# Performance work log

Measured on AMD Instinct MI355X. Metric: run time of the kernel, lower is better.

The kernel has to match this reference:

```python
import jax, jax.numpy as jnp
import numpy as np

N_BITS = 32
HIDDEN = 128


def _neighborhoods(z):
    """z: (B,k,H,W) -> (B,k,9,H,W) 3x3 neighborhoods (zero-padded), center zeroed.

    Position ordering matches F.unfold(kernel_size=3): row-major over (di,dj),
    so index 4 is the center, which the module masks to 0.
    """
    B, k, H, W = z.shape
    zp = jnp.pad(z, ((0, 0), (0, 0), (1, 1), (1, 1)))
    views = []
    for di in range(3):
        for dj in range(3):
            if di == 1 and dj == 1:  # center masked out
                views.append(jnp.zeros_like(z))
            else:
                views.append(zp[:, :, di:di + H, dj:dj + W])
    return jnp.stack(views, axis=2)  # (B,k,9,H,W)


def setup_inputs() -> dict:
    key = jax.random.key(0)
    k1, k2, k3, k4, k5 = jax.random.split(key, 5)
    B, k, H, W = 8, N_BITS, 256, 256
    z = jax.random.normal(k1, (B, k, H, W), dtype=jnp.float32)
    # nn.Linear(9*k, hidden): weight (hidden, 9k), feature order = k-outer, 9-inner
    W1 = jax.random.normal(k2, (HIDDEN, 9 * k), dtype=jnp.float32) * (1.0 / np.sqrt(9 * k))
    b1 = jax.random.normal(k3, (HIDDEN,), dtype=jnp.float32) * 0.01
    W2 = jax.random.normal(k4, (k, HIDDEN), dtype=jnp.float32) * (1.0 / np.sqrt(HIDDEN))
    b2 = jax.random.normal(k5, (k,), dtype=jnp.float32) * 0.01
    return {"z": z, "W1": W1, "b1": b1, "W2": W2, "b2": b2}


def reference(z, W1, b1, W2, b2):
    B, k, H, W = z.shape
    win = _neighborhoods(z)                      # (B,k,9,H,W)
    W1r = W1.reshape(HIDDEN, k, 9)               # split (9k) -> (k,9), k-outer
    h = jnp.einsum('bkphw,dkp->bdhw', win, W1r) + b1[None, :, None, None]
    h = jax.nn.relu(h)
    logits = jnp.einsum('bdhw,kd->bkhw', h, W2) + b2[None, :, None, None]
    return logits  # (B,k,H,W)
```

## Files before the change

kernel.cpp:

```cpp
#include <hip/hip_runtime.h>


#define KC 32
#define HH 256
#define WW 256
#define HID 128
#define YS 8
#define ZROW 2640

typedef __attribute__((ext_vector_type(8))) short short8;
typedef __attribute__((ext_vector_type(4))) float f32x4;

__device__ __forceinline__ unsigned short f2bf(float f) {
    union { float f; unsigned int i; } x; x.f = f;
    unsigned int r = x.i + 0x7FFFu + ((x.i >> 16) & 1u);
    return (unsigned short)(r >> 16);
}

__global__ void prep_weights(const float* __restrict__ w1,
                             const float* __restrict__ w2,
                             unsigned short* __restrict__ w1t,
                             unsigned short* __restrict__ w2t) {
    int i = blockIdx.x * 256 + threadIdx.x;
    if (i < 9 * HID * KC) {
        int c = i & 31;
        int d = (i >> 5) & 127;
        int p = i >> 12;
        w1t[i] = f2bf(w1[d * (9 * KC) + c * 9 + p]);
    } else if (i < 9 * HID * KC + KC * HID) {
        int j = i - 9 * HID * KC;
        w2t[j] = f2bf(w2[j]);
    }
}

__global__ __launch_bounds__(256) void local_pred_kernel(
    const float* __restrict__ zg,
    const unsigned short* __restrict__ w1t,
    const float* __restrict__ b1g,
    const unsigned short* __restrict__ w2t,
    const float* __restrict__ b2g,
    float* __restrict__ outg)
{
    __shared__ __attribute__((aligned(16))) unsigned short z_lds[3 * ZROW];
    __shared__ __attribute__((aligned(16))) unsigned short h_lds[64 * 136];

    const int tid = threadIdx.x;
    const int l   = tid & 63;
    const int o   = tid >> 6;
    const int bidx = blockIdx.x;
    const int x0 = (bidx & 3) << 6;
    const int y0 = ((bidx >> 2) & 31) * YS;
    const int b  = bidx >> 7;

    const int wave = tid >> 6;
    const int lane = tid & 63;
    const int lr = lane & 15;
    const int lq = lane >> 4;
    const int wm = wave >> 1;
    const int wn = wave & 1;

    const float* zb = zg + (size_t)b * KC * HH * WW;

    float bias1[4];
#pragma unroll
    for (int nt = 0; nt < 4; ++nt) bias1[nt] = b1g[wn * 64 + nt * 16 + lr];
    float bias2[2];
#pragma unroll
    for (int nt = 0; nt < 2; ++nt) bias2[nt] = b2g[nt * 16 + lr];
    short8 w2f[4][2];
#pragma unroll
    for (int k4 = 0; k4 < 4; ++k4)
#pragma unroll
        for (int nt = 0; nt < 2; ++nt)
            w2f[k4][nt] = *(const short8*)&w2t[(nt * 16 + lr) * HID + k4 * 32 + lq * 8];

    const int aoff0 = (wm * 32 + lr) * 40 + lq * 8;
    const int bbase = (wn * 64 + lr) * KC + lq * 8;
    const int m2    = wave * 16 + lr;

    const int ho    = tid >> 1;
    const int hside = tid & 1;
    const int hgx   = x0 - 1 + hside * 65;
    const bool hgx_ok = (unsigned)hgx < (unsigned)WW;

    int sA = (y0 + 2) % 3, sB = y0 % 3, sC = (y0 + 1) % 3;

    {
        int slots[3] = {sA, sB, sC};
#pragma unroll
        for (int dy = 0; dy < 3; ++dy) {
            int gy = y0 - 1 + dy;
            int slot = slots[dy];
            bool rowok = (unsigned)gy < (unsigned)HH;
            float m8[8];
            const float* p = zb + ((o * 8) * HH + gy) * WW + x0 + l;
#pragma unroll
            for (int j = 0; j < 8; ++j) m8[j] = rowok ? p[j * HH * WW] : 0.f;
            union { short8 s; unsigned int u[4]; } w;
            union { float f; unsigned int i; } uu[8];
#pragma unroll
            for (int j = 0; j < 8; ++j) uu[j].f = m8[j];
#pragma unroll
            for (int k = 0; k < 4; ++k)
                w.u[k] = __builtin_amdgcn_perm(uu[2 * k + 1].i, uu[2 * k].i, 0x07060302u);
            *(short8*)&z_lds[(slot * 66 + l + 1) * 40 + o * 8] = w.s;
            if (tid < 8) {
                bool ok = rowok && hgx_ok;
                float e8[8];
                const float* q = zb + ((ho * 8) * HH + gy) * WW + hgx;
#pragma unroll
                for (int j = 0; j < 8; ++j) e8[j] = ok ? q[j * HH * WW] : 0.f;
                union { short8 s; unsigned int u[4]; } we;
                union { float f; unsigned int i; } ue[8];
#pragma unroll
                for (int j = 0; j < 8; ++j) ue[j].f = e8[j];
#pragma unroll
                for (int k = 0; k < 4; ++k)
                    we.u[k] = __builtin_amdgcn_perm(ue[2 * k + 1].i, ue[2 * k].i, 0x07060302u);
                *(short8*)&z_lds[(slot * 66 + hside * 65) * 40 + ho * 8] = we.s;
            }
        }
    }

    const int tap_di[8] = {0, 0, 0, 1, 1, 2, 2, 2};
    const int tap_dj[8] = {0, 1, 2, 0, 2, 0, 1, 2};

    for (int r = 0; r < YS; ++r) {
        const int y = y0 + r;
        __syncthreads();

        f32x4 acc[2][4];
#pragma unroll
        for (int mt = 0; mt < 2; ++mt)
#pragma unroll
            for (int nt = 0; nt < 4; ++nt)
                acc[mt][nt] = (f32x4){0.f, 0.f, 0.f, 0.f};

        const int rowoff[3] = {sA * ZROW, sB * ZROW, sC * ZROW};
#pragma unroll
        for (int t = 0; t < 8; ++t) {
            const int di = tap_di[t], dj = tap_dj[t];
            const int abase = rowoff[di] + dj * 40 + aoff0;
            short8 afr[2];
            afr[0] = *(const short8*)&z_lds[abase];
            afr[1] = *(const short8*)&z_lds[abase + 16 * 40];
            const int p = di * 3 + dj;
#pragma unroll
            for (int nt = 0; nt < 4; ++nt) {
                short8 bfr = *(const short8*)&w1t[p * (HID * KC) + nt * 512 + bbase];
#pragma unroll
                for (int mt = 0; mt < 2; ++mt)
                    acc[mt][nt] = __builtin_amdgcn_mfma_f32_16x16x32_bf16(
                        afr[mt], bfr, acc[mt][nt], 0, 0, 0);
            }
        }

#pragma unroll
        for (int nt = 0; nt < 4; ++nt) {
            int d = wn * 64 + nt * 16 + lr;
#pragma unroll
            for (int mt = 0; mt < 2; ++mt) {
#pragma unroll
                for (int rr = 0; rr < 4; ++rr) {
                    float v = acc[mt][nt][rr] + bias1[nt];
                    v = v > 0.f ? v : 0.f;
                    int m = wm * 32 + mt * 16 + lq * 4 + rr;
                    h_lds[m * 136 + d] = f2bf(v);
                }
            }
        }
        __syncthreads();

        const bool dostage = (r < YS - 1);
        const int gy = y + 2;
        const bool rowok = dostage && ((unsigned)gy < (unsigned)HH);
        float m8[8], e8[8];
        {
            const float* p = zb + ((o * 8) * HH + gy) * WW + x0 + l;
#pragma unroll
            for (int j = 0; j < 8; ++j) m8[j] = rowok ? p[j * HH * WW] : 0.f;
            bool ok = rowok && hgx_ok && (tid < 8);
            const float* q = zb + ((ho * 8) * HH + gy) * WW + hgx;
#pragma unroll
            for (int j = 0; j < 8; ++j) e8[j] = ok ? q[j * HH * WW] : 0.f;
        }

        f32x4 acc2[2];
        acc2[0] = (f32x4){0.f, 0.f, 0.f, 0.f};
        acc2[1] = (f32x4){0.f, 0.f, 0.f, 0.f};
#pragma unroll
        for (int k4 = 0; k4 < 4; ++k4) {
            short8 afr = *(const short8*)&h_lds[m2 * 136 + k4 * 32 + lq * 8];
#pragma unroll
            for (int nt = 0; nt < 2; ++nt)
                acc2[nt] = __builtin_amdgcn_mfma_f32_16x16x32_bf16(afr, w2f[k4][nt],
                                                                   acc2[nt], 0, 0, 0);
        }

#pragma unroll
        for (int nt = 0; nt < 2; ++nt) {
            int kout = nt * 16 + lr;
            f32x4 pack;
#pragma unroll
            for (int rr = 0; rr < 4; ++rr) pack[rr] = acc2[nt][rr] + bias2[nt];
            int mb = wave * 16 + lq * 4;
            size_t off = ((size_t)(b * KC + kout) * HH + y) * WW + x0 + mb;
            *(f32x4*)&outg[off] = pack;
        }

        if (dostage) {
            union { short8 s; unsigned int u[4]; } w;
            union { float f; unsigned int i; } uu[8];
#pragma unroll
            for (int j = 0; j < 8; ++j) uu[j].f = m8[j];
#pragma unroll
            for (int k = 0; k < 4; ++k)
                w.u[k] = __builtin_amdgcn_perm(uu[2 * k + 1].i, uu[2 * k].i, 0x07060302u);
            *(short8*)&z_lds[(sA * 66 + l + 1) * 40 + o * 8] = w.s;
            if (tid < 8) {
                union { short8 s; unsigned int u[4]; } we;
                union { float f; unsigned int i; } ue[8];
#pragma unroll
                for (int j = 0; j < 8; ++j) ue[j].f = e8[j];
#pragma unroll
                for (int k = 0; k < 4; ++k)
                    we.u[k] = __builtin_amdgcn_perm(ue[2 * k + 1].i, ue[2 * k].i, 0x07060302u);
                *(short8*)&z_lds[(sA * 66 + hside * 65) * 40 + ho * 8] = we.s;
            }
        }
        int t0 = sA; sA = sB; sB = sC; sC = t0;
    }
}

extern "C" void kernel_launch(void* const* d_in, const int* in_sizes, int n_in,
                              void* d_out, int out_size, void* d_ws, size_t ws_size,
                              hipStream_t stream)
{
    const float* z  = (const float*)d_in[0];
    const float* W1 = (const float*)d_in[1];
    const float* b1 = (const float*)d_in[2];
    const float* W2 = (const float*)d_in[3];
    const float* b2 = (const float*)d_in[4];
    float* out = (float*)d_out;
    unsigned short* w1t = (unsigned short*)d_ws;
    unsigned short* w2t = (unsigned short*)d_ws + 9 * HID * KC;

    hipLaunchKernelGGL(prep_weights, dim3(160), dim3(256), 0, stream, W1, W2, w1t, w2t);
    hipLaunchKernelGGL(local_pred_kernel, dim3(8 * 4 * (HH / YS)), dim3(256), 0, stream,
                       z, w1t, b1, w2t, b2, out);
}
```

Measured before the change: 188.7 us.

## Prefetch rows two ahead with a 4-slot ring and preload halo columns

The z staging ring grows from three to four LDS slots. Each row's global loads are issued two rows ahead, in the middle of the loop, so they overlap the GEMM1 epilogue and GEMM2, and the slot rotation is fully unrolled. Halo column values for all later rows are loaded once up front into a small LDS buffer. The first GEMM is re-tiled so each wave owns 32 hidden units across all 64 pixels, which halves the B-fragment loads per wave. The change also adds custom barrier macros and launch_bounds(256,4), which raises register pressure and LDS use and may hurt occupancy.

```diff
diff --git a/kernel.cpp b/kernel.cpp
--- a/kernel.cpp
+++ b/kernel.cpp
@@ -11,10 +11,24 @@
 typedef __attribute__((ext_vector_type(8))) short short8;
 typedef __attribute__((ext_vector_type(4))) float f32x4;
 
+#define BARRIER() asm volatile("s_waitcnt lgkmcnt(0)\n\ts_barrier" ::: "memory")
+#define SCHED_FENCE() asm volatile("" ::: "memory")
+
 __device__ __forceinline__ unsigned short f2bf(float f) {
     union { float f; unsigned int i; } x; x.f = f;
     unsigned int r = x.i + 0x7FFFu + ((x.i >> 16) & 1u);
     return (unsigned short)(r >> 16);
+}
+
+__device__ __forceinline__ short8 pack8(const float* v) {
+    union { short8 s; unsigned int u[4]; } w;
+    union { float f; unsigned int i; } uu[8];
+#pragma unroll
+    for (int j = 0; j < 8; ++j) uu[j].f = v[j];
+#pragma unroll
+    for (int k = 0; k < 4; ++k)
+        w.u[k] = __builtin_amdgcn_perm(uu[2 * k + 1].i, uu[2 * k].i, 0x07060302u);
+    return w.s;
 }
 
 __global__ void prep_weights(const float* __restrict__ w1,
@@ -33,7 +47,7 @@
     }
 }
 
-__global__ __launch_bounds__(256) void local_pred_kernel(
+__global__ __launch_bounds__(256, 4) void local_pred_kernel(
     const float* __restrict__ zg,
     const unsigned short* __restrict__ w1t,
     const float* __restrict__ b1g,
@@ -41,30 +55,78 @@
     const float* __restrict__ b2g,
     float* __restrict__ outg)
 {
-    __shared__ __attribute__((aligned(16))) unsigned short z_lds[3 * ZROW];
+    __shared__ __attribute__((aligned(16))) unsigned short z_lds[4 * ZROW];
     __shared__ __attribute__((aligned(16))) unsigned short h_lds[64 * 136];
-
-    const int tid = threadIdx.x;
-    const int l   = tid & 63;
-    const int o   = tid >> 6;
+    __shared__ __attribute__((aligned(16))) unsigned short halo_lds[7 * 2 * 32];
+
+    const int tid  = threadIdx.x;
     const int bidx = blockIdx.x;
     const int x0 = (bidx & 3) << 6;
     const int y0 = ((bidx >> 2) & 31) * YS;
     const int b  = bidx >> 7;
 
+    const int l = tid & 63;
+    const int o = tid >> 6;
+
     const int wave = tid >> 6;
     const int lane = tid & 63;
     const int lr = lane & 15;
     const int lq = lane >> 4;
-    const int wm = wave >> 1;
-    const int wn = wave & 1;
 
     const float* zb = zg + (size_t)b * KC * HH * WW;
 
-    float bias1[4];
-#pragma unroll
-    for (int nt = 0; nt < 4; ++nt) bias1[nt] = b1g[wn * 64 + nt * 16 + lr];
-    float bias2[2];
+    float p8[3][8];
+#pragma unroll
+    for (int dy = 0; dy < 3; ++dy) {
+        const int gy = y0 - 1 + dy;
+        const bool ok = (unsigned)gy < (unsigned)HH;
+        const int gyc = ok ? gy : 0;
+        const float* p = zb + ((size_t)(o * 8) * HH + gyc) * WW + x0 + l;
+#pragma unroll
+        for (int j = 0; j < 8; ++j) p8[dy][j] = ok ? p[(size_t)j * HH * WW] : 0.f;
+    }
+    const int nhs = tid & 1, nho = (tid >> 1) & 3, nhd = tid >> 3;
+    float nh8[8];
+    {
+        const int gy = y0 - 1 + nhd;
+        const int gx = x0 - 1 + nhs * 65;
+        const bool ok = (tid < 24) && ((unsigned)gy < (unsigned)HH) &&
+                        ((unsigned)gx < (unsigned)WW);
+        const int gyc = ok ? gy : 0, gxc = ok ? gx : 0;
+        const float* q = zb + ((size_t)(nho * 8) * HH + gyc) * WW + gxc;
+#pragma unroll
+        for (int j = 0; j < 8; ++j) nh8[j] = ok ? q[(size_t)j * HH * WW] : 0.f;
+    }
+    const int fidx = tid - 64;
+    const int fhs = fidx & 1, fho = (fidx >> 1) & 3, fhr = fidx >> 3;
+    float fh8[8];
+    {
+        const int gy = y0 + 2 + fhr;
+        const int gx = x0 - 1 + fhs * 65;
+        const bool ok = (tid >= 64) && (tid < 120) && (gy < HH) &&
+                        ((unsigned)gx < (unsigned)WW);
+        const int gyc = ok ? gy : 0, gxc = ok ? gx : 0;
+        const float* q = zb + ((size_t)(fho * 8) * HH + gyc) * WW + gxc;
+#pragma unroll
+        for (int j = 0; j < 8; ++j) fh8[j] = ok ? q[(size_t)j * HH * WW] : 0.f;
+    }
+    float mv[2][8];
+    {
+        const float* p = zb + ((size_t)(o * 8) * HH + (y0 + 2)) * WW + x0 + l;
+#pragma unroll
+        for (int j = 0; j < 8; ++j) mv[0][j] = p[(size_t)j * HH * WW];
+    }
+#pragma unroll
+    for (int dy = 0; dy < 3; ++dy)
+        *(short8*)&z_lds[(dy * 66 + l + 1) * 40 + o * 8] = pack8(p8[dy]);
+    if (tid < 24)
+        *(short8*)&z_lds[(nhd * 66 + nhs * 65) * 40 + nho * 8] = pack8(nh8);
+    if (tid >= 64 && tid < 120)
+        *(short8*)&halo_lds[(fhr * 2 + fhs) * 32 + fho * 8] = pack8(fh8);
+
+    float bias1[2], bias2[2];
+#pragma unroll
+    for (int nt = 0; nt < 2; ++nt) bias1[nt] = b1g[wave * 32 + nt * 16 + lr];
 #pragma unroll
     for (int nt = 0; nt < 2; ++nt) bias2[nt] = b2g[nt * 16 + lr];
     short8 w2f[4][2];
@@ -74,161 +136,103 @@
         for (int nt = 0; nt < 2; ++nt)
             w2f[k4][nt] = *(const short8*)&w2t[(nt * 16 + lr) * HID + k4 * 32 + lq * 8];
 
-    const int aoff0 = (wm * 32 + lr) * 40 + lq * 8;
-    const int bbase = (wn * 64 + lr) * KC + lq * 8;
-    const int m2    = wave * 16 + lr;
-
-    const int ho    = tid >> 1;
-    const int hside = tid & 1;
-    const int hgx   = x0 - 1 + hside * 65;
-    const bool hgx_ok = (unsigned)hgx < (unsigned)WW;
-
-    int sA = (y0 + 2) % 3, sB = y0 % 3, sC = (y0 + 1) % 3;
-
-    {
-        int slots[3] = {sA, sB, sC};
-#pragma unroll
-        for (int dy = 0; dy < 3; ++dy) {
-            int gy = y0 - 1 + dy;
-            int slot = slots[dy];
-            bool rowok = (unsigned)gy < (unsigned)HH;
-            float m8[8];
-            const float* p = zb + ((o * 8) * HH + gy) * WW + x0 + l;
-#pragma unroll
-            for (int j = 0; j < 8; ++j) m8[j] = rowok ? p[j * HH * WW] : 0.f;
-            union { short8 s; unsigned int u[4]; } w;
-            union { float f; unsigned int i; } uu[8];
-#pragma unroll
-            for (int j = 0; j < 8; ++j) uu[j].f = m8[j];
-#pragma unroll
-            for (int k = 0; k < 4; ++k)
-                w.u[k] = __builtin_amdgcn_perm(uu[2 * k + 1].i, uu[2 * k].i, 0x07060302u);
-            *(short8*)&z_lds[(slot * 66 + l + 1) * 40 + o * 8] = w.s;
-            if (tid < 8) {
-                bool ok = rowok && hgx_ok;
-                float e8[8];
-                const float* q = zb + ((ho * 8) * HH + gy) * WW + hgx;
-#pragma unroll
-                for (int j = 0; j < 8; ++j) e8[j] = ok ? q[j * HH * WW] : 0.f;
-                union { short8 s; unsigned int u[4]; } we;
-                union { float f; unsigned int i; } ue[8];
-#pragma unroll
-                for (int j = 0; j < 8; ++j) ue[j].f = e8[j];
-#pragma unroll
-                for (int k = 0; k < 4; ++k)
-                    we.u[k] = __builtin_amdgcn_perm(ue[2 * k + 1].i, ue[2 * k].i, 0x07060302u);
-                *(short8*)&z_lds[(slot * 66 + hside * 65) * 40 + ho * 8] = we.s;
-            }
-        }
-    }
+    BARRIER();
 
     const int tap_di[8] = {0, 0, 0, 1, 1, 2, 2, 2};
     const int tap_dj[8] = {0, 1, 2, 0, 2, 0, 1, 2};
 
+#pragma unroll
     for (int r = 0; r < YS; ++r) {
         const int y = y0 + r;
-        __syncthreads();
-
-        f32x4 acc[2][4];
-#pragma unroll
-        for (int mt = 0; mt < 2; ++mt)
-#pragma unroll
-            for (int nt = 0; nt < 4; ++nt)
+        const int S0 = r & 3, S1 = (r + 1) & 3, S2 = (r + 2) & 3, S3 = (r + 3) & 3;
+
+        f32x4 acc[4][2];
+#pragma unroll
+        for (int mt = 0; mt < 4; ++mt)
+#pragma unroll
+            for (int nt = 0; nt < 2; ++nt)
                 acc[mt][nt] = (f32x4){0.f, 0.f, 0.f, 0.f};
 
-        const int rowoff[3] = {sA * ZROW, sB * ZROW, sC * ZROW};
+        const int rowoff[3] = {S0 * ZROW, S1 * ZROW, S2 * ZROW};
 #pragma unroll
         for (int t = 0; t < 8; ++t) {
             const int di = tap_di[t], dj = tap_dj[t];
-            const int abase = rowoff[di] + dj * 40 + aoff0;
-            short8 afr[2];
-            afr[0] = *(const short8*)&z_lds[abase];
-            afr[1] = *(const short8*)&z_lds[abase + 16 * 40];
             const int p = di * 3 + dj;
-#pragma unroll
-            for (int nt = 0; nt < 4; ++nt) {
-                short8 bfr = *(const short8*)&w1t[p * (HID * KC) + nt * 512 + bbase];
-#pragma unroll
-                for (int mt = 0; mt < 2; ++mt)
+            short8 afr[4];
+#pragma unroll
+            for (int mt = 0; mt < 4; ++mt)
+                afr[mt] = *(const short8*)&z_lds[rowoff[di] + (mt * 16 + lr + dj) * 40 + lq * 8];
+            short8 bfr[2];
+#pragma unroll
+            for (int nt = 0; nt < 2; ++nt)
+                bfr[nt] = *(const short8*)&w1t[p * (HID * KC) + (wave * 32 + nt * 16 + lr) * KC + lq * 8];
+#pragma unroll
+            for (int nt = 0; nt < 2; ++nt)
+#pragma unroll
+                for (int mt = 0; mt < 4; ++mt)
                     acc[mt][nt] = __builtin_amdgcn_mfma_f32_16x16x32_bf16(
-                        afr[mt], bfr, acc[mt][nt], 0, 0, 0);
-            }
-        }
-
-#pragma unroll
-        for (int nt = 0; nt < 4; ++nt) {
-            int d = wn * 64 + nt * 16 + lr;
-#pragma unroll
-            for (int mt = 0; mt < 2; ++mt) {
+                        afr[mt], bfr[nt], acc[mt][nt], 0, 0, 0);
+        }
+
+        SCHED_FENCE();
+        if (r < 6) {
+            const int gy = y + 3;
+            const bool ok = gy < HH;
+            const int gyc = ok ? gy : 0;
+            const float* p = zb + ((size_t)(o * 8) * HH + gyc) * WW + x0 + l;
+#pragma unroll
+            for (int j = 0; j < 8; ++j) mv[(r + 1) & 1][j] = ok ? p[(size_t)j * HH * WW] : 0.f;
+        }
+        SCHED_FENCE();
+
+#pragma unroll
+        for (int nt = 0; nt < 2; ++nt) {
+            const int d = wave * 32 + nt * 16 + lr;
+#pragma unroll
+            for (int mt = 0; mt < 4; ++mt)
 #pragma unroll
                 for (int rr = 0; rr < 4; ++rr) {
                     float v = acc[mt][nt][rr] + bias1[nt];
                     v = v > 0.f ? v : 0.f;
-                    int m = wm * 32 + mt * 16 + lq * 4 + rr;
+                    const int m = mt * 16 + lq * 4 + rr;
                     h_lds[m * 136 + d] = f2bf(v);
                 }
-            }
-        }
-        __syncthreads();
-
-        const bool dostage = (r < YS - 1);
-        const int gy = y + 2;
-        const bool rowok = dostage && ((unsigned)gy < (unsigned)HH);
-        float m8[8], e8[8];
-        {
-            const float* p = zb + ((o * 8) * HH + gy) * WW + x0 + l;
-#pragma unroll
-            for (int j = 0; j < 8; ++j) m8[j] = rowok ? p[j * HH * WW] : 0.f;
-            bool ok = rowok && hgx_ok && (tid < 8);
-            const float* q = zb + ((ho * 8) * HH + gy) * WW + hgx;
-#pragma unroll
-            for (int j = 0; j < 8; ++j) e8[j] = ok ? q[j * HH * WW] : 0.f;
-        }
+        }
+        BARRIER();
 
         f32x4 acc2[2];
         acc2[0] = (f32x4){0.f, 0.f, 0.f, 0.f};
         acc2[1] = (f32x4){0.f, 0.f, 0.f, 0.f};
+        const int m2 = wave * 16 + lr;
 #pragma unroll
         for (int k4 = 0; k4 < 4; ++k4) {
             short8 afr = *(const short8*)&h_lds[m2 * 136 + k4 * 32 + lq * 8];
 #pragma unroll
             for (int nt = 0; nt < 2; ++nt)
-                acc2[nt] = __builtin_amdgcn_mfma_f32_16x16x32_bf16(afr, w2f[k4][nt],
-                                                                   acc2[nt], 0, 0, 0);
+                acc2[nt] = __builtin_amdgcn_mfma_f32_16x16x32_bf16(
+                    afr, w2f[k4][nt], acc2[nt], 0, 0, 0);
         }
 
 #pragma unroll
         for (int nt = 0; nt < 2; ++nt) {
-            int kout = nt * 16 + lr;
-            f32x4 pack;
-#pragma unroll
-            for (int rr = 0; rr < 4; ++rr) pack[rr] = acc2[nt][rr] + bias2[nt];
-            int mb = wave * 16 + lq * 4;
-            size_t off = ((size_t)(b * KC + kout) * HH + y) * WW + x0 + mb;
-            *(f32x4*)&outg[off] = pack;
-        }
-
-        if (dostage) {
-            union { short8 s; unsigned int u[4]; } w;
-            union { float f; unsigned int i; } uu[8];
-#pragma unroll
-            for (int j = 0; j < 8; ++j) uu[j].f = m8[j];
-#pragma unroll
-            for (int k = 0; k < 4; ++k)
-                w.u[k] = __builtin_amdgcn_perm(uu[2 * k + 1].i, uu[2 * k].i, 0x07060302u);
-            *(short8*)&z_lds[(sA * 66 + l + 1) * 40 + o * 8] = w.s;
+            const int kout = nt * 16 + lr;
+            f32x4 pk;
+#pragma unroll
+            for (int rr = 0; rr < 4; ++rr) pk[rr] = acc2[nt][rr] + bias2[nt];
+            const int mb = wave * 16 + lq * 4;
+            const size_t off = ((size_t)(b * KC + kout) * HH + y) * WW + x0 + mb;
+            *(f32x4*)&outg[off] = pk;
+        }
+
+        if (r < 7) {
+            *(short8*)&z_lds[(S3 * 66 + l + 1) * 40 + o * 8] = pack8(mv[r & 1]);
             if (tid < 8) {
-                union { short8 s; unsigned int u[4]; } we;
-                union { float f; unsigned int i; } ue[8];
-#pragma unroll
-                for (int j = 0; j < 8; ++j) ue[j].f = e8[j];
-#pragma unroll
-                for (int k = 0; k < 4; ++k)
-                    we.u[k] = __builtin_amdgcn_perm(ue[2 * k + 1].i, ue[2 * k].i, 0x07060302u);
-                *(short8*)&z_lds[(sA * 66 + hside * 65) * 40 + ho * 8] = we.s;
+                const int side = tid & 1, oct = tid >> 1;
+                short8 hv = *(const short8*)&halo_lds[(r * 2 + side) * 32 + oct * 8];
+                *(short8*)&z_lds[(S3 * 66 + side * 65) * 40 + oct * 8] = hv;
             }
         }
-        int t0 = sA; sA = sB; sB = sC; sC = t0;
+        BARRIER();
     }
 }
 
```

Measured after the change: 210.5 us. +11.5%, slower.
